# Optimization experiments

Hardware: AMD Instinct MI355X
Metric: run time of the kernel (lower is better)

Reference implementation:

```python
import jax, jax.numpy as jnp
import numpy as np
from jax import lax

# dims
N_GRAPHS = 128
SEQ_LEN = 512          # nodes per graph (equal-length segments)
IN_DIM = 64
HIDDEN = 128
DEPTH = 3
KERNEL_LEN = 256       # klen = min(kernel_len, L) = 256 since L=512
LN_EPS = 1e-5


def setup_inputs() -> dict:
    key = jax.random.key(0)
    ks = jax.random.split(key, 10)
    N = N_GRAPHS * SEQ_LEN
    x = jax.random.normal(ks[0], (N, IN_DIM), dtype=jnp.float32)
    # equal-length contiguous segment ids: [0,0,...,1,1,...,B-1]
    batch = jnp.repeat(jnp.arange(N_GRAPHS, dtype=jnp.int32), SEQ_LEN)
    # in_proj Linear(in_dim -> hidden)
    W_proj = jax.random.normal(ks[1], (HIDDEN, IN_DIM), dtype=jnp.float32) / np.sqrt(IN_DIM)
    b_proj = jnp.zeros((HIDDEN,), dtype=jnp.float32)
    # per-block params, stacked over depth
    log_tau = jnp.full((DEPTH, HIDDEN), np.log(64.0), dtype=jnp.float32)
    W_in = jax.random.normal(ks[2], (DEPTH, 2 * HIDDEN, HIDDEN), dtype=jnp.float32) / np.sqrt(HIDDEN)
    b_in = jnp.zeros((DEPTH, 2 * HIDDEN), dtype=jnp.float32)
    W_out = jax.random.normal(ks[3], (DEPTH, HIDDEN, HIDDEN), dtype=jnp.float32) / np.sqrt(HIDDEN)
    b_out = jnp.zeros((DEPTH, HIDDEN), dtype=jnp.float32)
    gamma = jnp.ones((DEPTH, HIDDEN), dtype=jnp.float32)
    beta = jnp.zeros((DEPTH, HIDDEN), dtype=jnp.float32)
    return {"x": x, "batch": batch, "W_proj": W_proj, "b_proj": b_proj,
            "log_tau": log_tau, "W_in": W_in, "b_in": b_in,
            "W_out": W_out, "b_out": b_out, "gamma": gamma, "beta": beta}


def _lss_block(xb, log_tau_d, W_in_d, b_in_d, W_out_d, b_out_d, gamma_d, beta_d):
    # xb: (B, C, L)
    B, C, L = xb.shape
    K = min(KERNEL_LEN, L)
    t = jnp.arange(K, dtype=xb.dtype)
    tau = jnp.maximum(jnp.exp(log_tau_d), 0.001)[:, None]            # (C,1)
    k = jnp.exp(-t[None, :] / tau)                                   # (C,K)
    k = k / (k.sum(-1, keepdims=True) + 1e-8)
    w = k[:, None, :]                                                # (C,1,K)
    # causal depthwise conv1d (cross-correlation, left pad K-1), same as F.conv1d
    y = lax.conv_general_dilated(xb, w, window_strides=(1,),
                                 padding=[(K - 1, 0)],
                                 feature_group_count=C,
                                 dimension_numbers=("NCH", "OIH", "NCH"))
    y_t = y.transpose(0, 2, 1)                                       # (B,L,C)
    gates = y_t @ W_in_d.T + b_in_d                                  # (B,L,2C)
    a, g = jnp.split(gates, 2, axis=-1)
    y2 = (a * jax.nn.sigmoid(g)) @ W_out_d.T + b_out_d               # (B,L,C)
    z = y2 + y_t                                                     # residual (dropout is identity in eval)
    mu = z.mean(-1, keepdims=True)
    var = ((z - mu) ** 2).mean(-1, keepdims=True)
    out = (z - mu) / jnp.sqrt(var + LN_EPS) * gamma_d + beta_d
    return out.transpose(0, 2, 1)                                    # (B,C,L)


def reference(x, batch, W_proj, b_proj, log_tau, W_in, b_in, W_out, b_out, gamma, beta):
    N = x.shape[0]
    B = N // SEQ_LEN                                                 # equal-length segments
    h = x @ W_proj.T + b_proj                                        # (N,C) in_proj
    xb = h.reshape(B, SEQ_LEN, HIDDEN).transpose(0, 2, 1)            # (B,C,L)
    for d in range(DEPTH):
        xb = _lss_block(xb, log_tau[d], W_in[d], b_in[d], W_out[d], b_out[d], gamma[d], beta[d])
    return xb.mean(-1)                                               # (B, hidden)
```

## Files before the change

### kernel.cpp

```cpp
#include <hip/hip_runtime.h>
#include <stdint.h>
#include <stddef.h>

#define NG 128
#define SEQ 512
#define CIN 64
#define HID 128
#define NROWS (NG*SEQ)
#define KLEN 256
#define YS 272

typedef __attribute__((ext_vector_type(8))) short v8s;
typedef __attribute__((ext_vector_type(4))) short v4s;
typedef __attribute__((ext_vector_type(4))) float v4f;
typedef __attribute__((ext_vector_type(2))) unsigned v2u;
typedef unsigned short u16;

__device__ __forceinline__ float b2f(u16 u) {
    union { unsigned int i; float f; } v; v.i = ((unsigned int)u) << 16; return v.f;
}
__device__ __forceinline__ u16 f2b(float f) {
    unsigned int x = __float_as_uint(f);
    unsigned int r = (x + 0x7fffu + ((x >> 16) & 1u)) >> 16;
    return (u16)r;
}
__device__ __forceinline__ unsigned cvtpk(float lo, float hi) {
    unsigned r;
    asm("v_cvt_pk_bf16_f32 %0, %1, %2" : "=v"(r) : "v"(lo), "v"(hi));
    return r;
}
__device__ __forceinline__ float sigf(float x) { return 1.0f / (1.0f + __expf(-x)); }

__global__ void prep_kernel(const float* __restrict__ Wp, const float* __restrict__ Wi,
                            const float* __restrict__ Wo,
                            u16* __restrict__ Wpbf, u16* __restrict__ Wibf,
                            u16* __restrict__ Wobf) {
    int stride = gridDim.x * blockDim.x;
    int t0 = blockIdx.x * blockDim.x + threadIdx.x;
    for (int i = t0; i < 3 * 2 * HID * HID; i += stride) Wibf[i] = f2b(Wi[i]);
    for (int i = t0; i < 3 * HID * HID; i += stride) Wobf[i] = f2b(Wo[i]);
    for (int i = t0; i < HID * CIN; i += stride) Wpbf[i] = f2b(Wp[i]);
}

__global__ __launch_bounds__(256, 4) void proj_kernel(const float* __restrict__ x,
                                                      const u16* __restrict__ Wp,
                                                      const float* __restrict__ bp,
                                                      u16* __restrict__ actR) {
    const int wave = threadIdx.x >> 6, lane = threadIdx.x & 63;
    const int fr = lane & 15, kgrp = lane >> 4;
    const int l = blockIdx.x * 64 + wave * 16 + fr;
    const int n0 = kgrp * 4;

    v4f acc[8];
#pragma unroll
    for (int nt = 0; nt < 8; ++nt) acc[nt] = (v4f){0.f, 0.f, 0.f, 0.f};

#pragma unroll
    for (int ks = 0; ks < 2; ++ks) {
        const float* ap = x + (size_t)l * CIN + ks * 32 + kgrp * 8;
        float4 f0 = *(const float4*)ap;
        float4 f1 = *(const float4*)(ap + 4);
        union { unsigned u[4]; v8s s; } bf;
        bf.u[0] = cvtpk(f0.x, f0.y); bf.u[1] = cvtpk(f0.z, f0.w);
        bf.u[2] = cvtpk(f1.x, f1.y); bf.u[3] = cvtpk(f1.z, f1.w);
#pragma unroll
        for (int nt = 0; nt < 8; ++nt) {
            v8s a = *(const v8s*)(Wp + (size_t)(nt * 16 + fr) * CIN + ks * 32 + kgrp * 8);
            acc[nt] = __builtin_amdgcn_mfma_f32_16x16x32_bf16(a, bf.s, acc[nt], 0, 0, 0);
        }
    }
#pragma unroll
    for (int nt = 0; nt < 8; ++nt) {
        const int c = nt * 16 + n0;
        float4 bb = *(const float4*)(bp + c);
        union { unsigned u[2]; v4s s; } pk;
        pk.u[0] = cvtpk(acc[nt][0] + bb.x, acc[nt][1] + bb.y);
        pk.u[1] = cvtpk(acc[nt][2] + bb.z, acc[nt][3] + bb.w);
        *(v4s*)(actR + (size_t)l * HID + c) = pk.s;
    }
}

__global__ __launch_bounds__(512) void chunkh_kernel(const u16* __restrict__ actR,
                                                     float* __restrict__ Pre,
                                                     const float* __restrict__ log_tau, int d) {
    __shared__ float2 t8[8][64];
    const int tid = threadIdx.x;
    const int g = blockIdx.x;
    const int cp = tid & 63, sc = tid >> 6;
    const int c0 = 2 * cp;
    const unsigned* x32 = (const unsigned*)(actR + (size_t)g * (SEQ * HID));
    float q0, q1, sp0, sp1;
    {
        float tau0 = fmaxf(expf(log_tau[d * HID + c0]), 0.001f);
        float tau1 = fmaxf(expf(log_tau[d * HID + c0 + 1]), 0.001f);
        float lq0 = -(1.0f / tau0) * 1.44269504089f;
        float lq1 = -(1.0f / tau1) * 1.44269504089f;
        q0 = exp2f(lq0); q1 = exp2f(lq1);
        sp0 = exp2f((float)(sc * 64) * lq0);
        sp1 = exp2f((float)(sc * 64) * lq1);
    }
    float h0[8], h1[8];
#pragma unroll
    for (int s = 0; s < 8; ++s) {
        float a0 = 0.f, a1 = 0.f;
#pragma unroll
        for (int j = 0; j < 8; ++j) {
            unsigned xv = x32[(size_t)(sc * 64 + s * 8 + j) * 64 + cp];
            a0 += sp0 * b2f((u16)(xv & 0xffff));
            a1 += sp1 * b2f((u16)(xv >> 16));
            sp0 *= q0; sp1 *= q1;
        }
        h0[s] = a0; h1[s] = a1;
    }
    float T0 = 0.f, T1 = 0.f;
#pragma unroll
    for (int s = 0; s < 8; ++s) { T0 += h0[s]; T1 += h1[s]; }
    t8[sc][cp] = make_float2(T0, T1);
    __syncthreads();
    float b0 = 0.f, b1 = 0.f;
    for (int s = 0; s < sc; ++s) { float2 v = t8[s][cp]; b0 += v.x; b1 += v.y; }
    float* PreG = Pre + (size_t)g * 64 * HID;
#pragma unroll
    for (int s = 0; s < 8; ++s) {
        *(float2*)(PreG + (size_t)(sc * 8 + s) * HID + c0) = make_float2(b0, b1);
        b0 += h0[s]; b1 += h1[s];
    }
}

__global__ __launch_bounds__(512, 4) void fused_kernel(const u16* __restrict__ actR,
                                                       const float* __restrict__ Pre,
                                                       const u16* __restrict__ Win,
                                                       const u16* __restrict__ Wout,
                                                       const float* __restrict__ b_in,
                                                       const float* __restrict__ b_out,
                                                       const float* __restrict__ gamma,
                                                       const float* __restrict__ beta,
                                                       const float* __restrict__ log_tau, int d,
                                                       u16* __restrict__ actRout) {
    __shared__ __align__(16) char ylds[64 * YS];
    __shared__ __align__(16) char ulds[64 * YS];
    __shared__ float2 red[8][64];
    __shared__ float2 murstd[64];
    const int tid = threadIdx.x;
    const int g = blockIdx.x >> 3, tile = blockIdx.x & 7;
    const int r0 = tile * 64;
    const size_t gbase = (size_t)g * (SEQ * HID);

    {
        const int cp = tid & 63, sc = tid >> 6;
        const int c0 = 2 * cp;
        const int l0 = r0 + sc * 8;
        const bool hasd = (r0 >= KLEN);
        const unsigned* x32 = (const unsigned*)(actR + gbase);
        unsigned xw[8], xdw[8];
#pragma unroll
        for (int j = 0; j < 8; ++j) xw[j] = x32[(size_t)(l0 + j) * 64 + cp];
        if (hasd) {
#pragma unroll
            for (int j = 0; j < 8; ++j) xdw[j] = x32[(size_t)(l0 - KLEN + j) * 64 + cp];
        }
        const float* PreG = Pre + ((size_t)g * 64 + (l0 >> 3)) * HID + c0;
        float2 pin = *(const float2*)PreG;
        float2 pdin = hasd ? *(const float2*)(PreG - 32 * HID) : make_float2(0.f, 0.f);
        float P[2], Pd[2], sp[2], w[2], spd[2], q[2], qinv[2];
#pragma unroll
        for (int k = 0; k < 2; ++k) {
            float tau = fmaxf(expf(log_tau[d * HID + c0 + k]), 0.001f);
            float lq = -(1.0f / tau) * 1.44269504089f;
            q[k] = exp2f(lq);
            float S = (q[k] < 0.9999999f) ? (1.0f - exp2f(256.0f * lq)) / (1.0f - q[k]) : 256.0f;
            float invS = 1.0f / (S + 1e-8f);
            qinv[k] = exp2f(-lq);
            sp[k] = exp2f((float)l0 * lq);
            w[k] = exp2f((float)(255 - l0) * lq) * invS;
            spd[k] = hasd ? exp2f((float)(l0 - KLEN) * lq) : 0.f;
            P[k] = k ? pin.y : pin.x;
            Pd[k] = k ? pdin.y : pdin.x;
        }
#pragma unroll
        for (int j = 0; j < 8; ++j) {
            const int lt = sc * 8 + j;
            float y0, y1;
            {
                P[0] += sp[0] * b2f((u16)(xw[j] & 0xffff)); sp[0] *= q[0];
                P[1] += sp[1] * b2f((u16)(xw[j] >> 16));    sp[1] *= q[1];
                float Po0 = 0.f, Po1 = 0.f;
                if (hasd) {
                    Pd[0] += spd[0] * b2f((u16)(xdw[j] & 0xffff)); spd[0] *= q[0]; Po0 = Pd[0];
                    Pd[1] += spd[1] * b2f((u16)(xdw[j] >> 16));    spd[1] *= q[1]; Po1 = Pd[1];
                }
                y0 = w[0] * (P[0] - Po0); w[0] *= qinv[0];
                y1 = w[1] * (P[1] - Po1); w[1] *= qinv[1];
            }
            *(unsigned*)(ylds + lt * YS + ((4 * cp) ^ ((lt & 7) << 4))) = cvtpk(y0, y1);
        }
    }

    const int wave = tid >> 6, lane = tid & 63;
    const int fr = lane & 15, kgrp = lane >> 4;
    const int n0 = wave * 16 + kgrp * 4;

    v8s b1a[4], b1g[4], b2[4];
#pragma unroll
    for (int ks = 0; ks < 4; ++ks) {
        b1a[ks] = *(const v8s*)(Win + (size_t)(wave * 16 + fr) * HID + ks * 32 + kgrp * 8);
        b1g[ks] = *(const v8s*)(Win + (size_t)((wave + 8) * 16 + fr) * HID + ks * 32 + kgrp * 8);
        b2[ks]  = *(const v8s*)(Wout + (size_t)(wave * 16 + fr) * HID + ks * 32 + kgrp * 8);
    }
    const float4 ba4 = *(const float4*)(b_in + n0);
    const float4 bg4 = *(const float4*)(b_in + HID + n0);
    const float4 bo4 = *(const float4*)(b_out + n0);

    __syncthreads();

#pragma unroll
    for (int rt = 0; rt < 4; ++rt) {
        const int arow = rt * 16 + fr;
        const char* abase = ylds + arow * YS;
        const int asw = (arow & 7) << 4;
        v8s af[4];
#pragma unroll
        for (int ks = 0; ks < 4; ++ks)
            af[ks] = *(const v8s*)(abase + ((ks * 64 + kgrp * 16) ^ asw));
        v4f a0 = (v4f){0.f, 0.f, 0.f, 0.f}, a1 = (v4f){0.f, 0.f, 0.f, 0.f};
#pragma unroll
        for (int ks = 0; ks < 4; ++ks) {
            a0 = __builtin_amdgcn_mfma_f32_16x16x32_bf16(b1a[ks], af[ks], a0, 0, 0, 0);
            a1 = __builtin_amdgcn_mfma_f32_16x16x32_bf16(b1g[ks], af[ks], a1, 0, 0, 0);
        }
        float u0 = (a0[0] + ba4.x) * sigf(a1[0] + bg4.x);
        float u1 = (a0[1] + ba4.y) * sigf(a1[1] + bg4.y);
        float u2 = (a0[2] + ba4.z) * sigf(a1[2] + bg4.z);
        float u3 = (a0[3] + ba4.w) * sigf(a1[3] + bg4.w);
        v2u pk;
        pk[0] = cvtpk(u0, u1); pk[1] = cvtpk(u2, u3);
        *(v2u*)(ulds + arow * YS + ((2 * n0) ^ asw)) = pk;
    }
    __syncthreads();

    v4f acc2[4];
#pragma unroll
    for (int rt = 0; rt < 4; ++rt) acc2[rt] = (v4f){0.f, 0.f, 0.f, 0.f};
#pragma unroll
    for (int rt = 0; rt < 4; ++rt) {
        const int arow = rt * 16 + fr;
        const char* abase = ulds + arow * YS;
        const int asw = (arow & 7) << 4;
#pragma unroll
        for (int ks = 0; ks < 4; ++ks) {
            v8s af = *(const v8s*)(abase + ((ks * 64 + kgrp * 16) ^ asw));
            acc2[rt] = __builtin_amdgcn_mfma_f32_16x16x32_bf16(b2[ks], af, acc2[rt], 0, 0, 0);
        }
    }
#pragma unroll
    for (int rt = 0; rt < 4; ++rt) {
        const int l = rt * 16 + fr;
        v4s yv = *(const v4s*)(ylds + l * YS + ((2 * n0) ^ ((l & 7) << 4)));
        float z0 = acc2[rt][0] + bo4.x + b2f((u16)yv[0]);
        float z1 = acc2[rt][1] + bo4.y + b2f((u16)yv[1]);
        float z2 = acc2[rt][2] + bo4.z + b2f((u16)yv[2]);
        float z3 = acc2[rt][3] + bo4.w + b2f((u16)yv[3]);
        acc2[rt][0] = z0; acc2[rt][1] = z1; acc2[rt][2] = z2; acc2[rt][3] = z3;
        float s = z0 + z1 + z2 + z3;
        float sq = z0 * z0 + z1 * z1 + z2 * z2 + z3 * z3;
        s += __shfl_xor(s, 16); sq += __shfl_xor(sq, 16);
        s += __shfl_xor(s, 32); sq += __shfl_xor(sq, 32);
        if (lane < 16) red[wave][l] = make_float2(s, sq);
    }
    __syncthreads();

    if (tid < 64) {
        float a = 0.f, b = 0.f;
#pragma unroll
        for (int j = 0; j < 8; ++j) { float2 v = red[j][tid]; a += v.x; b += v.y; }
        float mu = a * (1.0f / 128.0f);
        float var = b * (1.0f / 128.0f) - mu * mu;
        murstd[tid] = make_float2(mu, rsqrtf(var + 1e-5f));
    }
    __syncthreads();

    const float4 gm4 = *(const float4*)(gamma + n0);
    const float4 bt4 = *(const float4*)(beta + n0);
#pragma unroll
    for (int rt = 0; rt < 4; ++rt) {
        const int l = rt * 16 + fr;
        float2 ms = murstd[l];
        float o0 = (acc2[rt][0] - ms.x) * ms.y * gm4.x + bt4.x;
        float o1 = (acc2[rt][1] - ms.x) * ms.y * gm4.y + bt4.y;
        float o2 = (acc2[rt][2] - ms.x) * ms.y * gm4.z + bt4.z;
        float o3 = (acc2[rt][3] - ms.x) * ms.y * gm4.w + bt4.w;
        union { unsigned u[2]; v4s s; } pk;
        pk.u[0] = cvtpk(o0, o1); pk.u[1] = cvtpk(o2, o3);
        *(v4s*)(actRout + gbase + (size_t)(r0 + l) * HID + n0) = pk.s;
    }
}

__global__ __launch_bounds__(512) void mean_kernel(const u16* __restrict__ actR, float* __restrict__ out) {
    __shared__ float2 red[8][64];
    const int tid = threadIdx.x;
    const int g = blockIdx.x;
    const int cp = tid & 63, lq8 = tid >> 6;
    const unsigned* x32 = (const unsigned*)(actR + (size_t)g * (SEQ * HID));
    float s0 = 0.f, s1 = 0.f;
#pragma unroll
    for (int j = 0; j < 64; ++j) {
        unsigned v = x32[(size_t)(lq8 * 64 + j) * 64 + cp];
        s0 += b2f((u16)(v & 0xffff));
        s1 += b2f((u16)(v >> 16));
    }
    red[lq8][cp] = make_float2(s0, s1);
    __syncthreads();
    if (tid < 64) {
        float a = 0.f, b = 0.f;
#pragma unroll
        for (int j = 0; j < 8; ++j) { float2 v = red[j][tid]; a += v.x; b += v.y; }
        *(float2*)(out + (size_t)g * HID + 2 * tid) =
            make_float2(a * (1.0f / 512.0f), b * (1.0f / 512.0f));
    }
}

extern "C" void kernel_launch(void* const* d_in, const int* in_sizes, int n_in,
                              void* d_out, int out_size, void* d_ws, size_t ws_size,
                              hipStream_t stream) {
    const float* x       = (const float*)d_in[0];
    const float* Wp      = (const float*)d_in[2];
    const float* bp      = (const float*)d_in[3];
    const float* log_tau = (const float*)d_in[4];
    const float* Wi      = (const float*)d_in[5];
    const float* bi      = (const float*)d_in[6];
    const float* Wo      = (const float*)d_in[7];
    const float* bo      = (const float*)d_in[8];
    const float* gm      = (const float*)d_in[9];
    const float* bt      = (const float*)d_in[10];
    float* out = (float*)d_out;

    char* ws = (char*)d_ws;
    const size_t ACT_BYTES = (size_t)NROWS * HID * 2;
    u16* actA   = (u16*)(ws);
    u16* actB   = (u16*)(ws + ACT_BYTES);
    float* Pre  = (float*)(ws + 2 * ACT_BYTES);
    char* wbase = ws + 2 * ACT_BYTES + (size_t)NG * 64 * HID * 4;
    u16* Wibf = (u16*)(wbase);
    u16* Wobf = (u16*)(wbase + (size_t)3 * 2 * HID * HID * 2);
    u16* Wpbf = (u16*)(wbase + (size_t)3 * 2 * HID * HID * 2 + (size_t)3 * HID * HID * 2);

    prep_kernel<<<128, 256, 0, stream>>>(Wp, Wi, Wo, Wpbf, Wibf, Wobf);
    proj_kernel<<<NROWS / 64, 256, 0, stream>>>(x, Wpbf, bp, actA);

    u16* cur = actA, *nxt = actB;
    for (int d = 0; d < 3; ++d) {
        chunkh_kernel<<<NG, 512, 0, stream>>>(cur, Pre, log_tau, d);
        fused_kernel<<<NG * 8, 512, 0, stream>>>(cur, Pre,
            Wibf + (size_t)d * 2 * HID * HID, Wobf + (size_t)d * HID * HID,
            bi + d * 2 * HID, bo + d * HID, gm + d * HID, bt + d * HID,
            log_tau, d, nxt);
        u16* t = cur; cur = nxt; nxt = t;
    }
    mean_kernel<<<NG, 512, 0, stream>>>(cur, out);
}
```

Measured before the change: 135.1 us.

## Precompute decay tables, fuse final mean into last block, widen chunk scan

Per-channel decay constants (log q, q, 1/q, 1/S) are computed once in the prep kernel and read from a table, instead of being recomputed with expf and divisions in every block. The last depth's fused kernel reduces its layer-norm output straight into per-tile column sums, which skips the final bf16 activation write and the full mean-kernel reread. A small kernel then finishes the mean. The chunk-prefix kernel moves to 1024 threads with shorter chunks, sigmoid uses the hardware exp2 and rcp instructions, the LDS row stride drops from 272 to 256, and occupancy bounds go up to 8 blocks. The smaller stride relies on the XOR swizzle to avoid bank conflicts, and the approximate rcp slightly changes numerics.

Result: slower. 191.9 us (+42.0%).

```diff
diff --git a/kernel.cpp b/kernel.cpp
--- a/kernel.cpp
+++ b/kernel.cpp
@@ -8,7 +8,7 @@
 #define HID 128
 #define NROWS (NG*SEQ)
 #define KLEN 256
-#define YS 272
+#define YS 256
 
 typedef __attribute__((ext_vector_type(8))) short v8s;
 typedef __attribute__((ext_vector_type(4))) short v4s;
@@ -29,17 +29,36 @@
     asm("v_cvt_pk_bf16_f32 %0, %1, %2" : "=v"(r) : "v"(lo), "v"(hi));
     return r;
 }
-__device__ __forceinline__ float sigf(float x) { return 1.0f / (1.0f + __expf(-x)); }
+__device__ __forceinline__ float exp2a(float x) {
+#if __has_builtin(__builtin_amdgcn_exp2f)
+    return __builtin_amdgcn_exp2f(x);
+#else
+    float r;
+    asm("v_exp_f32 %0, %1\n\ts_nop 1" : "=v"(r) : "v"(x));
+    return r;
+#endif
+}
+__device__ __forceinline__ float rcpa(float x) { return __builtin_amdgcn_rcpf(x); }
+__device__ __forceinline__ float sigf(float x) {
+    return rcpa(1.0f + exp2a(-x * 1.44269504089f));
+}
 
 __global__ void prep_kernel(const float* __restrict__ Wp, const float* __restrict__ Wi,
-                            const float* __restrict__ Wo,
+                            const float* __restrict__ Wo, const float* __restrict__ log_tau,
                             u16* __restrict__ Wpbf, u16* __restrict__ Wibf,
-                            u16* __restrict__ Wobf) {
+                            u16* __restrict__ Wobf, float4* __restrict__ tab) {
     int stride = gridDim.x * blockDim.x;
     int t0 = blockIdx.x * blockDim.x + threadIdx.x;
     for (int i = t0; i < 3 * 2 * HID * HID; i += stride) Wibf[i] = f2b(Wi[i]);
     for (int i = t0; i < 3 * HID * HID; i += stride) Wobf[i] = f2b(Wo[i]);
     for (int i = t0; i < HID * CIN; i += stride) Wpbf[i] = f2b(Wp[i]);
+    if (t0 < 3 * HID) {
+        float tau = fmaxf(expf(log_tau[t0]), 0.001f);
+        float q = expf(-1.0f / tau);
+        float lq = -(1.0f / tau) * 1.44269504089f;
+        float S = (q < 0.9999999f) ? (1.0f - exp2f(256.0f * lq)) / (1.0f - q) : 256.0f;
+        tab[t0] = make_float4(lq, q, exp2f(-lq), 1.0f / (S + 1e-8f));
+    }
 }
 
 __global__ __launch_bounds__(256, 4) void proj_kernel(const float* __restrict__ x,
@@ -80,54 +99,48 @@
     }
 }
 
-__global__ __launch_bounds__(512) void chunkh_kernel(const u16* __restrict__ actR,
-                                                     float* __restrict__ Pre,
-                                                     const float* __restrict__ log_tau, int d) {
-    __shared__ float2 t8[8][64];
+__global__ __launch_bounds__(1024) void chunkh_kernel(const u16* __restrict__ actR,
+                                                      float* __restrict__ Pre,
+                                                      const float4* __restrict__ tab) {
+    __shared__ float2 t16[16][64];
     const int tid = threadIdx.x;
     const int g = blockIdx.x;
     const int cp = tid & 63, sc = tid >> 6;
     const int c0 = 2 * cp;
+    const int l0 = sc * 32;
     const unsigned* x32 = (const unsigned*)(actR + (size_t)g * (SEQ * HID));
-    float q0, q1, sp0, sp1;
-    {
-        float tau0 = fmaxf(expf(log_tau[d * HID + c0]), 0.001f);
-        float tau1 = fmaxf(expf(log_tau[d * HID + c0 + 1]), 0.001f);
-        float lq0 = -(1.0f / tau0) * 1.44269504089f;
-        float lq1 = -(1.0f / tau1) * 1.44269504089f;
-        q0 = exp2f(lq0); q1 = exp2f(lq1);
-        sp0 = exp2f((float)(sc * 64) * lq0);
-        sp1 = exp2f((float)(sc * 64) * lq1);
-    }
-    float h0[8], h1[8];
-#pragma unroll
-    for (int s = 0; s < 8; ++s) {
+    float4 tv0 = tab[c0], tv1 = tab[c0 + 1];
+    float q0 = tv0.y, q1 = tv1.y;
+    float sp0 = exp2a((float)l0 * tv0.x);
+    float sp1 = exp2a((float)l0 * tv1.x);
+    float h0[4], h1[4];
+#pragma unroll
+    for (int k = 0; k < 4; ++k) {
         float a0 = 0.f, a1 = 0.f;
 #pragma unroll
         for (int j = 0; j < 8; ++j) {
-            unsigned xv = x32[(size_t)(sc * 64 + s * 8 + j) * 64 + cp];
+            unsigned xv = x32[(size_t)(l0 + k * 8 + j) * 64 + cp];
             a0 += sp0 * b2f((u16)(xv & 0xffff));
             a1 += sp1 * b2f((u16)(xv >> 16));
             sp0 *= q0; sp1 *= q1;
         }
-        h0[s] = a0; h1[s] = a1;
-    }
-    float T0 = 0.f, T1 = 0.f;
-#pragma unroll
-    for (int s = 0; s < 8; ++s) { T0 += h0[s]; T1 += h1[s]; }
-    t8[sc][cp] = make_float2(T0, T1);
+        h0[k] = a0; h1[k] = a1;
+    }
+    t16[sc][cp] = make_float2(h0[0] + h0[1] + h0[2] + h0[3],
+                              h1[0] + h1[1] + h1[2] + h1[3]);
     __syncthreads();
     float b0 = 0.f, b1 = 0.f;
-    for (int s = 0; s < sc; ++s) { float2 v = t8[s][cp]; b0 += v.x; b1 += v.y; }
+    for (int s = 0; s < sc; ++s) { float2 v = t16[s][cp]; b0 += v.x; b1 += v.y; }
     float* PreG = Pre + (size_t)g * 64 * HID;
 #pragma unroll
-    for (int s = 0; s < 8; ++s) {
-        *(float2*)(PreG + (size_t)(sc * 8 + s) * HID + c0) = make_float2(b0, b1);
-        b0 += h0[s]; b1 += h1[s];
-    }
-}
-
-__global__ __launch_bounds__(512, 4) void fused_kernel(const u16* __restrict__ actR,
+    for (int k = 0; k < 4; ++k) {
+        *(float2*)(PreG + (size_t)(sc * 4 + k) * HID + c0) = make_float2(b0, b1);
+        b0 += h0[k]; b1 += h1[k];
+    }
+}
+
+template<int LAST>
+__global__ __launch_bounds__(512, 8) void fused_kernel(const u16* __restrict__ actR,
                                                        const float* __restrict__ Pre,
                                                        const u16* __restrict__ Win,
                                                        const u16* __restrict__ Wout,
@@ -135,8 +148,9 @@
                                                        const float* __restrict__ b_out,
                                                        const float* __restrict__ gamma,
                                                        const float* __restrict__ beta,
-                                                       const float* __restrict__ log_tau, int d,
-                                                       u16* __restrict__ actRout) {
+                                                       const float4* __restrict__ tab,
+                                                       u16* __restrict__ actRout,
+                                                       float* __restrict__ meansP) {
     __shared__ __align__(16) char ylds[64 * YS];
     __shared__ __align__(16) char ulds[64 * YS];
     __shared__ float2 red[8][64];
@@ -162,36 +176,30 @@
         const float* PreG = Pre + ((size_t)g * 64 + (l0 >> 3)) * HID + c0;
         float2 pin = *(const float2*)PreG;
         float2 pdin = hasd ? *(const float2*)(PreG - 32 * HID) : make_float2(0.f, 0.f);
-        float P[2], Pd[2], sp[2], w[2], spd[2], q[2], qinv[2];
-#pragma unroll
-        for (int k = 0; k < 2; ++k) {
-            float tau = fmaxf(expf(log_tau[d * HID + c0 + k]), 0.001f);
-            float lq = -(1.0f / tau) * 1.44269504089f;
-            q[k] = exp2f(lq);
-            float S = (q[k] < 0.9999999f) ? (1.0f - exp2f(256.0f * lq)) / (1.0f - q[k]) : 256.0f;
-            float invS = 1.0f / (S + 1e-8f);
-            qinv[k] = exp2f(-lq);
-            sp[k] = exp2f((float)l0 * lq);
-            w[k] = exp2f((float)(255 - l0) * lq) * invS;
-            spd[k] = hasd ? exp2f((float)(l0 - KLEN) * lq) : 0.f;
-            P[k] = k ? pin.y : pin.x;
-            Pd[k] = k ? pdin.y : pdin.x;
-        }
+        float4 tv0 = tab[c0], tv1 = tab[c0 + 1];
+        float P[2]   = { pin.x, pin.y };
+        float Pd[2]  = { pdin.x, pdin.y };
+        float q[2]   = { tv0.y, tv1.y };
+        float qinv[2] = { tv0.z, tv1.z };
+        float sp[2], w[2], spd[2];
+        sp[0] = exp2a((float)l0 * tv0.x);
+        sp[1] = exp2a((float)l0 * tv1.x);
+        w[0] = exp2a((float)(255 - l0) * tv0.x) * tv0.w;
+        w[1] = exp2a((float)(255 - l0) * tv1.x) * tv1.w;
+        spd[0] = hasd ? exp2a((float)(l0 - KLEN) * tv0.x) : 0.f;
+        spd[1] = hasd ? exp2a((float)(l0 - KLEN) * tv1.x) : 0.f;
 #pragma unroll
         for (int j = 0; j < 8; ++j) {
             const int lt = sc * 8 + j;
-            float y0, y1;
-            {
-                P[0] += sp[0] * b2f((u16)(xw[j] & 0xffff)); sp[0] *= q[0];
-                P[1] += sp[1] * b2f((u16)(xw[j] >> 16));    sp[1] *= q[1];
-                float Po0 = 0.f, Po1 = 0.f;
-                if (hasd) {
-                    Pd[0] += spd[0] * b2f((u16)(xdw[j] & 0xffff)); spd[0] *= q[0]; Po0 = Pd[0];
-                    Pd[1] += spd[1] * b2f((u16)(xdw[j] >> 16));    spd[1] *= q[1]; Po1 = Pd[1];
-                }
-                y0 = w[0] * (P[0] - Po0); w[0] *= qinv[0];
-                y1 = w[1] * (P[1] - Po1); w[1] *= qinv[1];
+            P[0] += sp[0] * b2f((u16)(xw[j] & 0xffff)); sp[0] *= q[0];
+            P[1] += sp[1] * b2f((u16)(xw[j] >> 16));    sp[1] *= q[1];
+            float Po0 = 0.f, Po1 = 0.f;
+            if (hasd) {
+                Pd[0] += spd[0] * b2f((u16)(xdw[j] & 0xffff)); spd[0] *= q[0]; Po0 = Pd[0];
+                Pd[1] += spd[1] * b2f((u16)(xdw[j] >> 16));    spd[1] *= q[1]; Po1 = Pd[1];
             }
+            float y0 = w[0] * (P[0] - Po0); w[0] *= qinv[0];
+            float y1 = w[1] * (P[1] - Po1); w[1] *= qinv[1];
             *(unsigned*)(ylds + lt * YS + ((4 * cp) ^ ((lt & 7) << 4))) = cvtpk(y0, y1);
         }
     }
@@ -281,42 +289,49 @@
 
     const float4 gm4 = *(const float4*)(gamma + n0);
     const float4 bt4 = *(const float4*)(beta + n0);
-#pragma unroll
-    for (int rt = 0; rt < 4; ++rt) {
-        const int l = rt * 16 + fr;
-        float2 ms = murstd[l];
-        float o0 = (acc2[rt][0] - ms.x) * ms.y * gm4.x + bt4.x;
-        float o1 = (acc2[rt][1] - ms.x) * ms.y * gm4.y + bt4.y;
-        float o2 = (acc2[rt][2] - ms.x) * ms.y * gm4.z + bt4.z;
-        float o3 = (acc2[rt][3] - ms.x) * ms.y * gm4.w + bt4.w;
-        union { unsigned u[2]; v4s s; } pk;
-        pk.u[0] = cvtpk(o0, o1); pk.u[1] = cvtpk(o2, o3);
-        *(v4s*)(actRout + gbase + (size_t)(r0 + l) * HID + n0) = pk.s;
-    }
-}
-
-__global__ __launch_bounds__(512) void mean_kernel(const u16* __restrict__ actR, float* __restrict__ out) {
-    __shared__ float2 red[8][64];
-    const int tid = threadIdx.x;
-    const int g = blockIdx.x;
-    const int cp = tid & 63, lq8 = tid >> 6;
-    const unsigned* x32 = (const unsigned*)(actR + (size_t)g * (SEQ * HID));
-    float s0 = 0.f, s1 = 0.f;
-#pragma unroll
-    for (int j = 0; j < 64; ++j) {
-        unsigned v = x32[(size_t)(lq8 * 64 + j) * 64 + cp];
-        s0 += b2f((u16)(v & 0xffff));
-        s1 += b2f((u16)(v >> 16));
-    }
-    red[lq8][cp] = make_float2(s0, s1);
-    __syncthreads();
-    if (tid < 64) {
-        float a = 0.f, b = 0.f;
-#pragma unroll
-        for (int j = 0; j < 8; ++j) { float2 v = red[j][tid]; a += v.x; b += v.y; }
-        *(float2*)(out + (size_t)g * HID + 2 * tid) =
-            make_float2(a * (1.0f / 512.0f), b * (1.0f / 512.0f));
-    }
+    if (LAST) {
+        float cs0 = 0.f, cs1 = 0.f, cs2 = 0.f, cs3 = 0.f;
+#pragma unroll
+        for (int rt = 0; rt < 4; ++rt) {
+            const int l = rt * 16 + fr;
+            float2 ms = murstd[l];
+            cs0 += (acc2[rt][0] - ms.x) * ms.y * gm4.x + bt4.x;
+            cs1 += (acc2[rt][1] - ms.x) * ms.y * gm4.y + bt4.y;
+            cs2 += (acc2[rt][2] - ms.x) * ms.y * gm4.z + bt4.z;
+            cs3 += (acc2[rt][3] - ms.x) * ms.y * gm4.w + bt4.w;
+        }
+#pragma unroll
+        for (int m = 1; m < 16; m <<= 1) {
+            cs0 += __shfl_xor(cs0, m); cs1 += __shfl_xor(cs1, m);
+            cs2 += __shfl_xor(cs2, m); cs3 += __shfl_xor(cs3, m);
+        }
+        if (fr == 0)
+            *(float4*)(meansP + ((size_t)(g * 8 + tile)) * HID + n0) =
+                make_float4(cs0, cs1, cs2, cs3);
+    } else {
+#pragma unroll
+        for (int rt = 0; rt < 4; ++rt) {
+            const int l = rt * 16 + fr;
+            float2 ms = murstd[l];
+            float o0 = (acc2[rt][0] - ms.x) * ms.y * gm4.x + bt4.x;
+            float o1 = (acc2[rt][1] - ms.x) * ms.y * gm4.y + bt4.y;
+            float o2 = (acc2[rt][2] - ms.x) * ms.y * gm4.z + bt4.z;
+            float o3 = (acc2[rt][3] - ms.x) * ms.y * gm4.w + bt4.w;
+            union { unsigned u[2]; v4s s; } pk;
+            pk.u[0] = cvtpk(o0, o1); pk.u[1] = cvtpk(o2, o3);
+            *(v4s*)(actRout + gbase + (size_t)(r0 + l) * HID + n0) = pk.s;
+        }
+    }
+}
+
+__global__ __launch_bounds__(128) void meanf_kernel(const float* __restrict__ meansP,
+                                                    float* __restrict__ out) {
+    const int g = blockIdx.x, c = threadIdx.x;
+    const float* p = meansP + (size_t)g * 8 * HID + c;
+    float s = 0.f;
+#pragma unroll
+    for (int t = 0; t < 8; ++t) s += p[t * HID];
+    out[(size_t)g * HID + c] = s * (1.0f / 512.0f);
 }
 
 extern "C" void kernel_launch(void* const* d_in, const int* in_sizes, int n_in,
@@ -336,25 +351,35 @@
 
     char* ws = (char*)d_ws;
     const size_t ACT_BYTES = (size_t)NROWS * HID * 2;
-    u16* actA   = (u16*)(ws);
-    u16* actB   = (u16*)(ws + ACT_BYTES);
-    float* Pre  = (float*)(ws + 2 * ACT_BYTES);
-    char* wbase = ws + 2 * ACT_BYTES + (size_t)NG * 64 * HID * 4;
+    u16* actA    = (u16*)(ws);
+    u16* actB    = (u16*)(ws + ACT_BYTES);
+    float* Pre   = (float*)(ws + 2 * ACT_BYTES);
+    float* meansP = (float*)(ws + 2 * ACT_BYTES + (size_t)NG * 64 * HID * 4);
+    char* wbase  = ws + 2 * ACT_BYTES + (size_t)NG * 64 * HID * 4 + (size_t)NG * 8 * HID * 4;
     u16* Wibf = (u16*)(wbase);
     u16* Wobf = (u16*)(wbase + (size_t)3 * 2 * HID * HID * 2);
     u16* Wpbf = (u16*)(wbase + (size_t)3 * 2 * HID * HID * 2 + (size_t)3 * HID * HID * 2);
-
-    prep_kernel<<<128, 256, 0, stream>>>(Wp, Wi, Wo, Wpbf, Wibf, Wobf);
+    float4* tab = (float4*)(wbase + (size_t)3 * 2 * HID * HID * 2 + (size_t)3 * HID * HID * 2
+                            + (size_t)HID * CIN * 2 + 64);
+
+    prep_kernel<<<128, 256, 0, stream>>>(Wp, Wi, Wo, log_tau, Wpbf, Wibf, Wobf, tab);
     proj_kernel<<<NROWS / 64, 256, 0, stream>>>(x, Wpbf, bp, actA);
 
     u16* cur = actA, *nxt = actB;
     for (int d = 0; d < 3; ++d) {
-        chunkh_kernel<<<NG, 512, 0, stream>>>(cur, Pre, log_tau, d);
-        fused_kernel<<<NG * 8, 512, 0, stream>>>(cur, Pre,
-            Wibf + (size_t)d * 2 * HID * HID, Wobf + (size_t)d * HID * HID,
-            bi + d * 2 * HID, bo + d * HID, gm + d * HID, bt + d * HID,
-            log_tau, d, nxt);
+        chunkh_kernel<<<NG, 1024, 0, stream>>>(cur, Pre, tab + (size_t)d * HID);
+        if (d < 2) {
+            fused_kernel<0><<<NG * 8, 512, 0, stream>>>(cur, Pre,
+                Wibf + (size_t)d * 2 * HID * HID, Wobf + (size_t)d * HID * HID,
+                bi + d * 2 * HID, bo + d * HID, gm + d * HID, bt + d * HID,
+                tab + (size_t)d * HID, nxt, nullptr);
+        } else {
+            fused_kernel<1><<<NG * 8, 512, 0, stream>>>(cur, Pre,
+                Wibf + (size_t)d * 2 * HID * HID, Wobf + (size_t)d * HID * HID,
+                bi + d * 2 * HID, bo + d * HID, gm + d * HID, bt + d * HID,
+                tab + (size_t)d * HID, nullptr, meansP);
+        }
         u16* t = cur; cur = nxt; nxt = t;
     }
-    mean_kernel<<<NG, 512, 0, stream>>>(cur, out);
-}
+    meanf_kernel<<<NG, 128, 0, stream>>>(meansP, out);
+}
```
